# Kernel optimization log

Hardware: AMD Instinct MI355X
Metric: run time of the kernel (lower is better)

Reference implementation:

```python
import jax, jax.numpy as jnp
import numpy as np

L = 512          # label_size (incl. START, STOP)
D = 2048         # 2 * rnn_hidden
T = 8192         # sequence length
START_ID = 510
STOP_ID = 511
NEG = -10000.0


def setup_inputs() -> dict:
    key = jax.random.key(0)
    k1, k2, k3, k4, k5 = jax.random.split(key, 5)
    x = jax.random.normal(k1, (1, T, D), dtype=jnp.float32)
    tags = jax.random.randint(k2, (T,), 0, START_ID)  # gold tags, never START/STOP
    W = jax.random.normal(k3, (D, L), dtype=jnp.float32) * 0.02
    b = jnp.zeros((L,), dtype=jnp.float32)
    transitions = jax.random.normal(k4, (L, L), dtype=jnp.float32)
    # replicate the constructor masking: no transition INTO START, none OUT OF STOP
    transitions = transitions.at[START_ID, :].set(NEG)
    transitions = transitions.at[:, STOP_ID].set(NEG)
    return {"x": x, "W": W, "b": b, "transitions": transitions,
            "tags": tags, "start_id": START_ID, "stop_id": STOP_ID}


def reference(x, W, b, transitions, tags, start_id, stop_id):
    # feats: [T, L] emission scores (batch squeezed, as in the torch code)
    feats = x[0] @ W + b

    # ---- forward algorithm (log-partition) as a scan over time ----
    init_alpha = jnp.full((L,), NEG, dtype=feats.dtype).at[start_id].set(0.0)

    def step(alpha, feat_t):
        # alpha_next[j] = feat_t[j] + logsumexp_i(alpha[i] + transitions[j, i])
        alpha_next = feat_t + jax.nn.logsumexp(alpha[None, :] + transitions, axis=1)
        return alpha_next, None

    alpha, _ = jax.lax.scan(step, init_alpha, feats)
    forward_score = jax.nn.logsumexp(alpha + transitions[stop_id])

    # ---- gold path score ----
    tags_ext = jnp.concatenate([jnp.array([start_id], dtype=tags.dtype), tags])
    trans_score = transitions[tags_ext[1:], tags_ext[:-1]].sum()
    emit_score = feats[jnp.arange(T), tags].sum()
    gold_score = trans_score + emit_score + transitions[stop_id, tags[-1]]

    nll = forward_score - gold_score  # neg_log_likelihood of the module
    return nll
```

## Files before the change

### kernel.cpp

```cpp
#include <hip/hip_runtime.h>

#define L 512
#define D 2048
#define T 8192

#define NCHUNK 4096
#define SCHUNK 2
#define WARM   3
#define STEPS  (WARM + SCHUNK)
#define NBLK   256
#define LOG256 5.545177444479562f

typedef __attribute__((ext_vector_type(8))) short bf16x8;
typedef __attribute__((ext_vector_type(4))) float f32x4;

static __device__ __forceinline__ unsigned short f2bf(float f) {
    unsigned u = __float_as_uint(f);
    unsigned r = ((u >> 16) & 1u) + 0x7fffu;
    return (unsigned short)((u + r) >> 16);
}
static __device__ __forceinline__ float bf2f(unsigned short h) {
    return __uint_as_float(((unsigned)h) << 16);
}

static __device__ __forceinline__ unsigned char f2fp8(float f) {
    unsigned u = __float_as_uint(f);
    u += ((u >> 20) & 1u) + 0x7FFFFu;
    int Ef = (int)((u >> 23) & 0xFF) - 120;
    unsigned M = (u >> 20) & 7u;
    if (Ef <= 0) return 0;
    if (Ef > 15) { Ef = 15; M = 7; }
    return (unsigned char)((Ef << 3) | M);
}
static __device__ __forceinline__ float fp8dec(unsigned char b) {
    const int Ef = (b >> 3) & 15;
    const int M  = b & 7;
    if (Ef == 0) return (float)M * 0.001953125f;
    return __uint_as_float((unsigned)(((Ef + 120) << 23) | (M << 20)));
}
static __device__ __forceinline__ unsigned pack4sw(float a, float b, float c, float d) {
    return (unsigned)f2fp8(a) | ((unsigned)f2fp8(b) << 8)
         | ((unsigned)f2fp8(c) << 16) | ((unsigned)f2fp8(d) << 24);
}
template <bool HI>
static __device__ __forceinline__ unsigned pk8(float a, float b, unsigned old) {
#if __has_builtin(__builtin_amdgcn_cvt_pk_fp8_f32)
    return __builtin_amdgcn_cvt_pk_fp8_f32(a, b, old, HI);
#else
    unsigned lo2 = (unsigned)f2fp8(fabsf(a)) | ((unsigned)f2fp8(fabsf(b)) << 8);
    return HI ? ((old & 0xFFFFu) | (lo2 << 16)) : ((old & 0xFFFF0000u) | lo2);
#endif
}
static __device__ __forceinline__ unsigned pack4hw(float a, float b, float c, float d) {
    return pk8<true>(c, d, pk8<false>(a, b, 0u));
}

static __device__ __forceinline__ void gll16(const void* g, void* l) {
    __builtin_amdgcn_global_load_lds(
        (const __attribute__((address_space(1))) void*)g,
        (__attribute__((address_space(3))) void*)l, 16, 0, 0);
}

#define XQ_BLOCKS ((T * D) / (256 * 8))
#define E8_BLOCKS ((L * L) / 256)
#define WQ_BLOCKS ((D / 64) * (L / 64))
__global__ __launch_bounds__(256) void prep(const float* __restrict__ x,
                                            const float* __restrict__ W,
                                            const float* __restrict__ trans,
                                            unsigned char* __restrict__ xq,
                                            unsigned char* __restrict__ Wq,
                                            unsigned char* __restrict__ E8) {
    __shared__ float tile[64][65];
    const int bid = blockIdx.x;
    const int tid = threadIdx.x;
    if (bid < XQ_BLOCKS) {
        const size_t i = ((size_t)bid * 256 + tid) * 8;
        const float4 a = *(const float4*)&x[i];
        const float4 c = *(const float4*)&x[i + 4];
        uint2 o;
        o.x = pk8<true>(a.z, a.w, pk8<false>(a.x, a.y, 0u));
        o.y = pk8<true>(c.z, c.w, pk8<false>(c.x, c.y, 0u));
        *(uint2*)&xq[i] = o;
    } else if (bid < XQ_BLOCKS + E8_BLOCKS) {
        const int i = (bid - XQ_BLOCKS) * 256 + tid;
        E8[i] = f2fp8(fminf(__expf(trans[i]), 448.0f));
    } else {
        const int rb = bid - XQ_BLOCKS - E8_BLOCKS;
        const int k0 = (rb & 31) * 64;
        const int n0 = (rb >> 5) * 64;
        const int r = tid >> 4, c4 = (tid & 15) * 4;
#pragma unroll
        for (int i = 0; i < 4; ++i) {
            const float4 v = *(const float4*)&W[(size_t)(k0 + r + i * 16) * L + n0 + c4];
            tile[r + i * 16][c4 + 0] = v.x;
            tile[r + i * 16][c4 + 1] = v.y;
            tile[r + i * 16][c4 + 2] = v.z;
            tile[r + i * 16][c4 + 3] = v.w;
        }
        __syncthreads();
#pragma unroll
        for (int i = 0; i < 4; ++i) {
            const int nn = r + i * 16;
            const unsigned p = pk8<true>(tile[c4 + 2][nn], tile[c4 + 3][nn],
                                         pk8<false>(tile[c4 + 0][nn], tile[c4 + 1][nn], 0u));
            *(unsigned*)&Wq[(size_t)(n0 + nn) * D + k0 + c4] = p;
        }
    }
}

__global__ __launch_bounds__(256) void gemm_ef(const unsigned char* __restrict__ xq,
                                               const unsigned char* __restrict__ Wq,
                                               const float* __restrict__ b,
                                               unsigned short* __restrict__ efb) {
    __shared__ __align__(16) unsigned char As[2][4096];
    __shared__ __align__(16) unsigned char Bs[2][8192];
    const int tid  = threadIdx.x;
    const int lane = tid & 63;
    const int wave = tid >> 6;
    const int bid  = blockIdx.x;
    const int slot = bid >> 3;
    const int brow = (bid & 7) + 8 * (slot >> 2);
    const int bcol = slot & 3;
    const int bm = brow * 64;
    const int bn = bcol * 128;
    const int wr = (wave >> 1) * 32;
    const int wc = (wave & 1) * 64;
    const int ln = lane & 15;
    const int g2 = lane >> 4;

    const int arow = wave * 16 + (lane >> 2);
    const int asq  = (lane & 3) ^ ((arow >> 1) & 3);
    const size_t asrc = (size_t)(bm + arow) * D + asq * 16;
    const int adst = wave * 1024;
    const int ldstB = wave * 1024;

    const int qsw = (ln >> 1) & 3;
    const int q0 = (((g2 >> 1) ^ qsw) << 4) | ((g2 & 1) * 8);
    const int q1 = (((2 + (g2 >> 1)) ^ qsw) << 4) | ((g2 & 1) * 8);

    f32x4 acc[2][4] = {};

    gll16(&xq[asrc], As[0] + adst);
#pragma unroll
    for (int j = 0; j < 2; ++j) {
        const int c = j * 256 + wave * 64 + lane;
        const int brw = c >> 2;
        const int bq  = (c & 3) ^ ((brw >> 1) & 3);
        gll16(&Wq[(size_t)(bn + brw) * D + bq * 16], Bs[0] + j * 4096 + ldstB);
    }
    __syncthreads();

    for (int kt = 0; kt < 32; ++kt) {
        const int cb = kt & 1;
        if (kt < 31) {
            const int k1 = (kt + 1) * 64;
            gll16(&xq[asrc + k1], As[cb ^ 1] + adst);
#pragma unroll
            for (int j = 0; j < 2; ++j) {
                const int c = j * 256 + wave * 64 + lane;
                const int brw = c >> 2;
                const int bq  = (c & 3) ^ ((brw >> 1) & 3);
                gll16(&Wq[(size_t)(bn + brw) * D + k1 + bq * 16],
                      Bs[cb ^ 1] + j * 4096 + ldstB);
            }
        }
#pragma unroll
        for (int kb = 0; kb < 2; ++kb) {
            const int qo = kb ? q1 : q0;
            long af[2], bfr[4];
#pragma unroll
            for (int m = 0; m < 2; ++m)
                af[m] = *(const long*)(As[cb] + (wr + m * 16 + ln) * 64 + qo);
#pragma unroll
            for (int n = 0; n < 4; ++n)
                bfr[n] = *(const long*)(Bs[cb] + (wc + n * 16 + ln) * 64 + qo);
#pragma unroll
            for (int m = 0; m < 2; ++m)
#pragma unroll
                for (int n = 0; n < 4; ++n)
                    acc[m][n] = __builtin_amdgcn_mfma_f32_16x16x32_fp8_fp8(
                        af[m], bfr[n], acc[m][n], 0, 0, 0);
        }
        __syncthreads();
    }
#pragma unroll
    for (int n = 0; n < 4; ++n) {
        const int col = bn + wc + n * 16 + ln;
        const float bias = b[col];
#pragma unroll
        for (int m = 0; m < 2; ++m) {
            const int rowb = bm + wr + m * 16 + g2 * 4;
#pragma unroll
            for (int r = 0; r < 4; ++r)
                efb[(size_t)(rowb + r) * L + col] = f2bf(__expf(acc[m][n][r] + bias));
        }
    }
}

__global__ __launch_bounds__(512, 2) void crf_scan(const unsigned char* __restrict__ E8,
                                                   const unsigned short* __restrict__ efb,
                                                   const float* __restrict__ trans,
                                                   const int* __restrict__ startp,
                                                   const int* __restrict__ stopp,
                                                   const int* __restrict__ tags,
                                                   float* __restrict__ partials,
                                                   float* __restrict__ gold4) {
    __shared__ __align__(16) unsigned char Elds[256 * 512];
    __shared__ __align__(16) unsigned char U8[16 * 512];
    __shared__ float wredf[128];
    __shared__ float tailred[8];

    const int tid  = threadIdx.x;
    const int lane = tid & 63;
    const int wave = tid >> 6;
    const int n    = lane & 15;
    const int g2   = lane >> 4;

    if (blockIdx.x >= NBLK) {
        const int blk = blockIdx.x - NBLK;
        const int startId = *startp;
        const int stopId  = *stopp;
        const int t0 = blk * (T / 4), t1 = t0 + (T / 4);
        float acc = 0.0f;
        for (int t = t0 + tid; t < t1; t += 512) {
            const int cur  = tags[t];
            const int prev = (t == 0) ? startId : tags[t - 1];
            acc += __logf(bf2f(efb[(size_t)t * L + cur])) + trans[(size_t)cur * L + prev];
            if (t == T - 1) acc += trans[(size_t)stopId * L + cur];
        }
#pragma unroll
        for (int s = 32; s; s >>= 1) acc += __shfl_xor(acc, s, 64);
        if (lane == 0) wredf[wave] = acc;
        __syncthreads();
        if (tid == 0) {
            float g = 0.0f;
            for (int w = 0; w < 8; ++w) g += wredf[w];
            gold4[blk] = g;
        }
        return;
    }

    const int sid = *startp;

#pragma unroll
    for (int it = 0; it < 16; ++it) {
        const int c    = it * 512 + tid;
        const int rowL = c >> 5;
        const int s16  = c & 31;
        const int rowG = 64 * (rowL >> 5) + 32 + ((rowL >> 4) & 1) * 16 + (rowL & 15);
        gll16(E8 + (size_t)rowG * 512 + (((s16 * 2) ^ (rowL & 14)) * 8),
              Elds + c * 16);
    }

    for (int nn = 0; nn < 16; ++nn) {
        float val = 1.0f;
        if (blockIdx.x == 0 && nn == 0) val = (tid == sid) ? 256.0f : 0.0f;
        U8[nn * 512 + ((((tid >> 3) ^ nn) << 3) | (tid & 7))] = f2fp8(val);
    }

    unsigned long long Areg[32];
#pragma unroll
    for (int m = 0; m < 2; ++m) {
        const unsigned char* ab = E8 + (size_t)(64 * wave + 16 * m + n) * L + g2 * 8;
#pragma unroll
        for (int kb = 0; kb < 16; ++kb)
            Areg[m * 16 + kb] = *(const unsigned long long*)(ab + kb * 32);
    }
#pragma unroll
    for (int i = 0; i < 32; ++i)
        asm volatile("" : "+a"(Areg[i]));
    __syncthreads();

    const int c0  = blockIdx.x * 16;
    const int tn0 = SCHUNK * (c0 + n) - WARM;

    int wb[4];
#pragma unroll
    for (int m = 0; m < 4; ++m) {
        const int q0 = 8 * wave + 2 * m + (g2 >> 1);
        wb[m] = n * 512 + (((q0 ^ n) << 3) | ((g2 & 1) * 4));
    }
    const int eA = (wave * 32 + n) * 512;
    const int eB = (wave * 32 + 16 + n) * 512;
    const int nsw = (n & 14) << 3;

    ushort4 ev[4];
    {
        const int tc = tn0 < 0 ? 0 : tn0;
#pragma unroll
        for (int m = 0; m < 4; ++m)
            ev[m] = *(const ushort4*)&efb[(size_t)tc * L + 64 * wave + 16 * m + 4 * g2];
    }

    float logZ = 0.0f;
    for (int s = 0; s < STEPS; ++s) {
        const int tn = tn0 + s;
        ushort4 evn[4];
        {
            int tnn = tn + 1;
            tnn = tnn < 0 ? 0 : (tnn >= T ? T - 1 : tnn);
#pragma unroll
            for (int m = 0; m < 4; ++m)
                evn[m] = *(const ushort4*)&efb[(size_t)tnn * L + 64 * wave + 16 * m + 4 * g2];
        }

        f32x4 acc[4] = {};
#pragma unroll
        for (int kb = 0; kb < 16; ++kb) {
            const long bfr = *(const long*)&U8[n * 512 + (((kb * 4 + g2) ^ n) << 3)];
            const int ko = ((kb * 4 + g2) << 3) ^ nsw;
            const long af2 = *(const long*)&Elds[eA + ko];
            const long af3 = *(const long*)&Elds[eB + ko];
            asm volatile("v_mfma_f32_16x16x32_fp8_fp8 %0, %1, %2, %0"
                         : "+v"(acc[0]) : "a"(Areg[kb]), "v"(bfr));
            asm volatile("v_mfma_f32_16x16x32_fp8_fp8 %0, %1, %2, %0"
                         : "+v"(acc[1]) : "a"(Areg[16 + kb]), "v"(bfr));
            acc[2] = __builtin_amdgcn_mfma_f32_16x16x32_fp8_fp8(af2, bfr, acc[2], 0, 0, 0);
            acc[3] = __builtin_amdgcn_mfma_f32_16x16x32_fp8_fp8(af3, bfr, acc[3], 0, 0, 0);
        }
        f32x4 wv[4];
        float lmax = 0.0f;
#pragma unroll
        for (int m = 0; m < 4; ++m) {
            wv[m][0] = acc[m][0] * bf2f(ev[m].x);
            wv[m][1] = acc[m][1] * bf2f(ev[m].y);
            wv[m][2] = acc[m][2] * bf2f(ev[m].z);
            wv[m][3] = acc[m][3] * bf2f(ev[m].w);
            lmax = fmaxf(lmax, fmaxf(fmaxf(wv[m][0], wv[m][1]), fmaxf(wv[m][2], wv[m][3])));
        }
        lmax = fmaxf(lmax, __shfl_xor(lmax, 16, 64));
        lmax = fmaxf(lmax, __shfl_xor(lmax, 32, 64));
        if (g2 == 0) wredf[wave * 16 + n] = lmax;
        __syncthreads();
        float mn = wredf[n];
#pragma unroll
        for (int w = 1; w < 8; ++w) mn = fmaxf(mn, wredf[w * 16 + n]);
        const float inv = 256.0f / mn;
        if (tn >= 0) {
            if (s >= WARM - 1) {
#pragma unroll
                for (int m = 0; m < 4; ++m)
                    *(unsigned*)&U8[wb[m]] = pack4sw(wv[m][0] * inv, wv[m][1] * inv,
                                                     wv[m][2] * inv, wv[m][3] * inv);
            } else {
#pragma unroll
                for (int m = 0; m < 4; ++m)
                    *(unsigned*)&U8[wb[m]] = pack4hw(wv[m][0] * inv, wv[m][1] * inv,
                                                     wv[m][2] * inv, wv[m][3] * inv);
            }
        }
        if (s >= WARM) logZ += __logf(mn);
        __syncthreads();
#pragma unroll
        for (int m = 0; m < 4; ++m) ev[m] = evn[m];
    }

    if (wave == 0 && g2 == 0) {
        const float pz = logZ - SCHUNK * LOG256;
        const bool isLast = (blockIdx.x == NBLK - 1) && (n == 15);
        if (!isLast) partials[c0 + n] = pz;
        else wredf[127] = pz;
    }
    __syncthreads();
    if (blockIdx.x == NBLK - 1) {
        const int st = *stopp;
        const int j = tid;
        const unsigned char ub = U8[15 * 512 + ((((j >> 3) ^ 15) << 3) | (j & 7))];
        float sv = fp8dec(ub) * 0.00390625f * __expf(trans[(size_t)st * L + j]);
#pragma unroll
        for (int msk = 1; msk <= 32; msk <<= 1) sv += __shfl_xor(sv, msk, 64);
        if (lane == 0) tailred[wave] = sv;
        __syncthreads();
        if (tid == 0) {
            float tot = 0.0f;
            for (int w = 0; w < 8; ++w) tot += tailred[w];
            partials[NCHUNK - 1] = wredf[127] + __logf(tot);
        }
    }
}

__global__ __launch_bounds__(256) void combine(const float* __restrict__ partials,
                                               const float* __restrict__ gold4,
                                               float* __restrict__ out) {
    __shared__ float red[4];
    const int tid = threadIdx.x;
    float s = 0.0f;
    for (int i = tid; i < NCHUNK; i += 256) s += partials[i];
#pragma unroll
    for (int m = 32; m; m >>= 1) s += __shfl_xor(s, m, 64);
    if ((tid & 63) == 0) red[tid >> 6] = s;
    __syncthreads();
    if (tid == 0)
        out[0] = red[0] + red[1] + red[2] + red[3]
               - (gold4[0] + gold4[1] + gold4[2] + gold4[3]);
}

extern "C" void kernel_launch(void* const* d_in, const int* in_sizes, int n_in,
                              void* d_out, int out_size, void* d_ws, size_t ws_size,
                              hipStream_t stream) {
    const float* x      = (const float*)d_in[0];
    const float* W      = (const float*)d_in[1];
    const float* b      = (const float*)d_in[2];
    const float* trans  = (const float*)d_in[3];
    const int*   tags   = (const int*)d_in[4];
    const int*   startp = (const int*)d_in[5];
    const int*   stopp  = (const int*)d_in[6];

    char* wsb = (char*)d_ws;
    size_t off = 0;
    unsigned short* efb = (unsigned short*)(wsb + off); off += (size_t)T * L * 2;
    unsigned char*  E8  = (unsigned char*)(wsb + off);  off += (size_t)L * L;
    unsigned char*  Wq  = (unsigned char*)(wsb + off);  off += (size_t)L * D;
    unsigned char*  xq  = (unsigned char*)(wsb + off);  off += (size_t)T * D;
    float* partials     = (float*)(wsb + off);          off += (size_t)NCHUNK * 4;
    float* gold4        = (float*)(wsb + off);
    float* out = (float*)d_out;

    prep<<<XQ_BLOCKS + E8_BLOCKS + WQ_BLOCKS, 256, 0, stream>>>(x, W, trans, xq, Wq, E8);
    gemm_ef<<<512, 256, 0, stream>>>(xq, Wq, b, efb);
    crf_scan<<<NBLK + 4, 512, 0, stream>>>(E8, efb, trans, startp, stopp, tags,
                                           partials, gold4);
    combine<<<1, 256, 0, stream>>>(partials, gold4, out);
}
```

Measured before the change: 76.09 us.

## Fuse x fp8 quantization into GEMM A-tile load path

Removes the separate prep pass that converts x to fp8 and writes an xq buffer; the GEMM now streams fp32 x tiles directly into LDS (with an XOR swizzle) and converts them to fp8 in registers before the MFMA. This drops one full read and write pass over x (64MB read plus 16MB write and re-read). In exchange the GEMM's A traffic grows fourfold, LDS use grows to 16KB per A stage, and the inner loop gains conversion work, since each A element is reconverted by each column-block that reads it.

Measured after the change: 83.99 us. 1.1x slower.

```diff
diff --git a/kernel.cpp b/kernel.cpp
--- a/kernel.cpp
+++ b/kernel.cpp
@@ -61,31 +61,20 @@
         (__attribute__((address_space(3))) void*)l, 16, 0, 0);
 }
 
-#define XQ_BLOCKS ((T * D) / (256 * 8))
 #define E8_BLOCKS ((L * L) / 256)
 #define WQ_BLOCKS ((D / 64) * (L / 64))
-__global__ __launch_bounds__(256) void prep(const float* __restrict__ x,
-                                            const float* __restrict__ W,
+__global__ __launch_bounds__(256) void prep(const float* __restrict__ W,
                                             const float* __restrict__ trans,
-                                            unsigned char* __restrict__ xq,
                                             unsigned char* __restrict__ Wq,
                                             unsigned char* __restrict__ E8) {
     __shared__ float tile[64][65];
     const int bid = blockIdx.x;
     const int tid = threadIdx.x;
-    if (bid < XQ_BLOCKS) {
-        const size_t i = ((size_t)bid * 256 + tid) * 8;
-        const float4 a = *(const float4*)&x[i];
-        const float4 c = *(const float4*)&x[i + 4];
-        uint2 o;
-        o.x = pk8<true>(a.z, a.w, pk8<false>(a.x, a.y, 0u));
-        o.y = pk8<true>(c.z, c.w, pk8<false>(c.x, c.y, 0u));
-        *(uint2*)&xq[i] = o;
-    } else if (bid < XQ_BLOCKS + E8_BLOCKS) {
-        const int i = (bid - XQ_BLOCKS) * 256 + tid;
+    if (bid < E8_BLOCKS) {
+        const int i = bid * 256 + tid;
         E8[i] = f2fp8(fminf(__expf(trans[i]), 448.0f));
     } else {
-        const int rb = bid - XQ_BLOCKS - E8_BLOCKS;
+        const int rb = bid - E8_BLOCKS;
         const int k0 = (rb & 31) * 64;
         const int n0 = (rb >> 5) * 64;
         const int r = tid >> 4, c4 = (tid & 15) * 4;
@@ -108,11 +97,11 @@
     }
 }
 
-__global__ __launch_bounds__(256) void gemm_ef(const unsigned char* __restrict__ xq,
+__global__ __launch_bounds__(256) void gemm_ef(const float* __restrict__ x,
                                                const unsigned char* __restrict__ Wq,
                                                const float* __restrict__ b,
                                                unsigned short* __restrict__ efb) {
-    __shared__ __align__(16) unsigned char As[2][4096];
+    __shared__ __align__(16) unsigned char As[2][16384];
     __shared__ __align__(16) unsigned char Bs[2][8192];
     const int tid  = threadIdx.x;
     const int lane = tid & 63;
@@ -128,10 +117,8 @@
     const int ln = lane & 15;
     const int g2 = lane >> 4;
 
-    const int arow = wave * 16 + (lane >> 2);
-    const int asq  = (lane & 3) ^ ((arow >> 1) & 3);
-    const size_t asrc = (size_t)(bm + arow) * D + asq * 16;
-    const int adst = wave * 1024;
+    const int arow = tid >> 4;
+    const int aq   = (tid & 15);
     const int ldstB = wave * 1024;
 
     const int qsw = (ln >> 1) & 3;
@@ -140,7 +127,12 @@
 
     f32x4 acc[2][4] = {};
 
-    gll16(&xq[asrc], As[0] + adst);
+#pragma unroll
+    for (int j = 0; j < 4; ++j) {
+        const int row = j * 16 + (tid >> 4);
+        gll16(&x[(size_t)(bm + row) * D + (aq ^ (row & 15)) * 4],
+              As[0] + (j * 256 + (tid >> 4) * 16) * 16);
+    }
 #pragma unroll
     for (int j = 0; j < 2; ++j) {
         const int c = j * 256 + wave * 64 + lane;
@@ -154,7 +146,12 @@
         const int cb = kt & 1;
         if (kt < 31) {
             const int k1 = (kt + 1) * 64;
-            gll16(&xq[asrc + k1], As[cb ^ 1] + adst);
+#pragma unroll
+            for (int j = 0; j < 4; ++j) {
+                const int row = j * 16 + (tid >> 4);
+                gll16(&x[(size_t)(bm + row) * D + k1 + (aq ^ (row & 15)) * 4],
+                      As[cb ^ 1] + (j * 256 + (tid >> 4) * 16) * 16);
+            }
 #pragma unroll
             for (int j = 0; j < 2; ++j) {
                 const int c = j * 256 + wave * 64 + lane;
@@ -167,10 +164,19 @@
 #pragma unroll
         for (int kb = 0; kb < 2; ++kb) {
             const int qo = kb ? q1 : q0;
-            long af[2], bfr[4];
-#pragma unroll
-            for (int m = 0; m < 2; ++m)
-                af[m] = *(const long*)(As[cb] + (wr + m * 16 + ln) * 64 + qo);
+            long af[2];
+#pragma unroll
+            for (int m = 0; m < 2; ++m) {
+                const int row = wr + m * 16 + ln;
+                const int rowb = row * 256;
+                const int s0 = kb * 8 + g2 * 2;
+                const f32x4 a0 = *(const f32x4*)(As[cb] + rowb + ((s0 ^ ln) << 4));
+                const f32x4 a1 = *(const f32x4*)(As[cb] + rowb + (((s0 + 1) ^ ln) << 4));
+                const unsigned w0 = pk8<true>(a0[2], a0[3], pk8<false>(a0[0], a0[1], 0u));
+                const unsigned w1 = pk8<true>(a1[2], a1[3], pk8<false>(a1[0], a1[1], 0u));
+                af[m] = (long)(((unsigned long long)w1 << 32) | w0);
+            }
+            long bfr[4];
 #pragma unroll
             for (int n = 0; n < 4; ++n)
                 bfr[n] = *(const long*)(Bs[cb] + (wc + n * 16 + ln) * 64 + qo);
@@ -411,13 +417,12 @@
     unsigned short* efb = (unsigned short*)(wsb + off); off += (size_t)T * L * 2;
     unsigned char*  E8  = (unsigned char*)(wsb + off);  off += (size_t)L * L;
     unsigned char*  Wq  = (unsigned char*)(wsb + off);  off += (size_t)L * D;
-    unsigned char*  xq  = (unsigned char*)(wsb + off);  off += (size_t)T * D;
     float* partials     = (float*)(wsb + off);          off += (size_t)NCHUNK * 4;
     float* gold4        = (float*)(wsb + off);
     float* out = (float*)d_out;
 
-    prep<<<XQ_BLOCKS + E8_BLOCKS + WQ_BLOCKS, 256, 0, stream>>>(x, W, trans, xq, Wq, E8);
-    gemm_ef<<<512, 256, 0, stream>>>(xq, Wq, b, efb);
+    prep<<<E8_BLOCKS + WQ_BLOCKS, 256, 0, stream>>>(W, trans, Wq, E8);
+    gemm_ef<<<512, 256, 0, stream>>>(x, Wq, b, efb);
     crf_scan<<<NBLK + 4, 512, 0, stream>>>(E8, efb, trans, startp, stopp, tags,
                                            partials, gold4);
     combine<<<1, 256, 0, stream>>>(partials, gold4, out);
```
